# Optimization experiments

Measured on AMD Instinct MI355X. Metric: run time of the kernel, lower is better.

Reference implementation:

```python
import jax, jax.numpy as jnp
from jax import lax
import numpy as np

EPS_BN = 1e-5


def _convT(x, w, b, s, p):
    # PyTorch ConvTranspose2d(w: (Cin,Cout,k,k)) as gradient-of-conv.
    k = w.shape[2]
    wf = jnp.flip(w, (2, 3)).transpose(1, 0, 2, 3)  # (Cout,Cin,k,k)
    y = lax.conv_general_dilated(x, wf, (1, 1), [(k - 1 - p, k - 1 - p)] * 2,
                                 lhs_dilation=(s, s),
                                 dimension_numbers=('NCHW', 'OIHW', 'NCHW'))
    return y + b[None, :, None, None]


def _bn_relu(x, g, b):
    # BatchNorm2d in training mode (batch stats, biased var) + ReLU
    m = x.mean((0, 2, 3), keepdims=True)
    v = x.var((0, 2, 3), keepdims=True)
    return jax.nn.relu(g[None, :, None, None] * (x - m) * lax.rsqrt(v + EPS_BN) + b[None, :, None, None])


def _sn(w, u):
    # One power iteration (detached, as in the torch SpectralNorm impl), sigma through live w.
    wm = w.reshape(w.shape[0], -1)
    wd = lax.stop_gradient(wm)
    v = wd.T @ u
    v = v / (jnp.linalg.norm(v) + 1e-12)
    un = wd @ v
    un = un / (jnp.linalg.norm(un) + 1e-12)
    sigma = un @ (wm @ v)
    return w / sigma


def _self_attn(x, wf, bf, wg, bg, wh, bh, gamma):
    # Faithful math of Self_Attn, but without materializing the (b,C,N^2,N^2) repeat.
    b_, C, f, _ = x.shape
    N = f * f
    k = C // 8
    fx = (jnp.einsum('bchw,oc->bohw', x, wf) + bf[None, :, None, None]).reshape(b_, k, N, f, f)
    gx = (jnp.einsum('bchw,oc->bohw', x, wg) + bg[None, :, None, None]).reshape(b_, k, N, f, f)
    hx = (jnp.einsum('bchw,oc->bohw', x, wh) + bh[None, :, None, None]).reshape(b_, C, N)
    # attn_dist[b,i,a,c] = sum_k f_view[b,k,i,c,a] * g_view[b,k,i,a,c]  (f spatially transposed)
    logits = jnp.einsum('bkica,bkiac->biac', fx, gx).reshape(b_, N, N)
    attn = jax.nn.softmax(logits, axis=-1)  # (b, N, N)
    out = jnp.einsum('bcj,bij->bci', hx, attn).reshape(b_, C, f, f)
    return gamma[0] * out + x, attn[:, None]


def setup_inputs() -> dict:
    key = jax.random.key(0)
    ks = iter(jax.random.split(key, 64))

    def rn(shape, s=0.02):
        return jax.random.normal(next(ks), shape, jnp.float32) * s

    def uvec(n):
        u = jax.random.normal(next(ks), (n,), jnp.float32)
        return u / jnp.linalg.norm(u)

    B, Z = 4, 100
    d = {'z': jax.random.normal(next(ks), (B, Z), jnp.float32)}
    d.update(w1=rn((Z, 512, 4, 4)), b1=jnp.zeros(512), u1=uvec(Z), g1=jnp.ones(512), be1=jnp.zeros(512))
    d.update(w2=rn((512, 256, 4, 4)), b2=jnp.zeros(256), u2=uvec(512), g2=jnp.ones(256), be2=jnp.zeros(256))
    d.update(w3=rn((256, 128, 4, 4)), b3=jnp.zeros(128), u3=uvec(256), g3=jnp.ones(128), be3=jnp.zeros(128))
    d.update(w4=rn((128, 64, 4, 4)), b4=jnp.zeros(64), u4=uvec(128), g4=jnp.ones(64), be4=jnp.zeros(64))
    d.update(wl=rn((64, 3, 4, 4)), bl=jnp.zeros(3))
    d.update(wf1=rn((4096, 128)), bf1=jnp.zeros(4096), wg1=rn((4096, 128)), bg1=jnp.zeros(4096),
             wh1=rn((128, 128)), bh1=jnp.zeros(128), gamma1=jnp.full((1,), 0.5, jnp.float32))
    d.update(wf2=rn((8192, 64)), bf2=jnp.zeros(8192), wg2=rn((8192, 64)), bg2=jnp.zeros(8192),
             wh2=rn((64, 64)), bh2=jnp.zeros(64), gamma2=jnp.full((1,), 0.5, jnp.float32))
    return d


def reference(z, w1, b1, u1, g1, be1, w2, b2, u2, g2, be2, w3, b3, u3, g3, be3,
              w4, b4, u4, g4, be4, wl, bl,
              wf1, bf1, wg1, bg1, wh1, bh1, gamma1,
              wf2, bf2, wg2, bg2, wh2, bh2, gamma2):
    x = z[:, :, None, None]                                   # (B,100,1,1)
    x = _bn_relu(_convT(x, _sn(w1, u1), b1, 1, 0), g1, be1)   # (B,512,4,4)
    x = _bn_relu(_convT(x, _sn(w2, u2), b2, 2, 1), g2, be2)   # (B,256,8,8)
    x = _bn_relu(_convT(x, _sn(w3, u3), b3, 2, 1), g3, be3)   # (B,128,16,16)
    x, p1 = _self_attn(x, wf1, bf1, wg1, bg1, wh1, bh1, gamma1)
    x = _bn_relu(_convT(x, _sn(w4, u4), b4, 2, 1), g4, be4)   # (B,64,32,32)
    x, p2 = _self_attn(x, wf2, bf2, wg2, bg2, wh2, bh2, gamma2)
    out = jnp.tanh(_convT(x, wl, bl, 2, 1))                   # (B,3,64,64)
    return out, p1, p2
```

## Files before the change

kernel.cpp:

```cpp
#include <hip/hip_runtime.h>
#include <math.h>

#define DEV __device__ __forceinline__
typedef unsigned short ushort;
typedef __attribute__((ext_vector_type(8))) short bf16x8;
typedef __attribute__((ext_vector_type(4))) float f32x4;

constexpr int ACC   = 0;
constexpr int VR1   = 16;
constexpr int VR2   = VR1 + 8192;
constexpr int VR3   = VR2 + 4096;
constexpr int VR4   = VR3 + 2048;
constexpr int WS_Y1  = 16384;
constexpr int WS_Y2  = WS_Y1 + 32768;
constexpr int WS_Y3  = WS_Y2 + 65536;
constexpr int WS_BF3 = WS_Y3 + 131072;
constexpr int WS_H1T = WS_BF3 + 131072;
constexpr int WS_X3B = WS_H1T + 131072;
constexpr int WS_Y4  = WS_X3B + 131072;
constexpr int WS_BF4 = WS_Y4 + 262144;
constexpr int WS_H2T = WS_BF4 + 262144;
constexpr int WS_X4B = WS_H2T + 262144;
constexpr int WS_WB  = WS_X4B + 262144;
constexpr int WS_PART= WS_WB + 1048576;
constexpr int WS_WT2 = WS_PART + 1048576;
constexpr int WS_WT3 = WS_WT2 + 2097152;
constexpr int WS_WT4 = WS_WT3 + 524288;
constexpr int WS_WTL = WS_WT4 + 131072;

constexpr int O_P1 = 49152;
constexpr int O_P2 = O_P1 + 262144;

DEV ushort f2bf(float v){
  unsigned b = __float_as_uint(v);
  return (ushort)((b + 0x7fffu + ((b >> 16) & 1u)) >> 16);
}
DEV float wave_sum(float v){
  #pragma unroll
  for (int o = 32; o; o >>= 1) v += __shfl_xor(v, o, 64);
  return v;
}
DEV float wave_max(float v){
  #pragma unroll
  for (int o = 32; o; o >>= 1) v = fmaxf(v, __shfl_xor(v, o, 64));
  return v;
}
template<int T>
DEV float block_sum(float v, float* sm){
  v = wave_sum(v);
  if (T == 64) return v;
  __syncthreads();
  if ((threadIdx.x & 63) == 0) sm[threadIdx.x >> 6] = v;
  __syncthreads();
  float r = 0.f;
  #pragma unroll
  for (int i = 0; i < T/64; ++i) r += sm[i];
  return r;
}
template<int T>
DEV float block_max(float v, float* sm){
  v = wave_max(v);
  if (T == 64) return v;
  __syncthreads();
  if ((threadIdx.x & 63) == 0) sm[threadIdx.x >> 6] = v;
  __syncthreads();
  float r = -INFINITY;
  #pragma unroll
  for (int i = 0; i < T/64; ++i) r = fmaxf(r, sm[i]);
  return r;
}

DEV float inv_sigma(const float* __restrict__ ws, int wi){
  float d1 = sqrtf(ws[ACC + wi]) + 1e-12f;
  float s2 = ws[ACC + 4 + wi] / (d1 * d1);
  float sig = s2 / (sqrtf(s2) + 1e-12f);
  return 1.0f / sig;
}

__global__ void zero_vr_k(float* ws){
  int tid = blockIdx.x * 256 + threadIdx.x;
  ws[VR1 + tid] = 0.f;
  if (blockIdx.x == 0 && threadIdx.x < 8) ws[ACC + threadIdx.x] = 0.f;
}

__global__ void sn1_k(const float* __restrict__ w1, const float* __restrict__ w2,
                      const float* __restrict__ w3, const float* __restrict__ w4,
                      const float* __restrict__ u1, const float* __restrict__ u2,
                      const float* __restrict__ u3, const float* __restrict__ u4,
                      float* __restrict__ ws){
  int gid = blockIdx.x * 256 + threadIdx.x;
  int col_g = gid % 15360;
  int rchunk = gid / 15360;
  const float* W; const float* U; int rows, cols, col, voff;
  if (col_g < 8192)       { W=w1; U=u1; rows=100; cols=8192; col=col_g;        voff=VR1; }
  else if (col_g < 12288) { W=w2; U=u2; rows=512; cols=4096; col=col_g-8192;   voff=VR2; }
  else if (col_g < 14336) { W=w3; U=u3; rows=256; cols=2048; col=col_g-12288;  voff=VR3; }
  else                    { W=w4; U=u4; rows=128; cols=1024; col=col_g-14336;  voff=VR4; }
  int rc = rows >> 2;
  int r0 = rchunk * rc, r1 = r0 + rc;
  float a0=0.f, a1=0.f, a2=0.f, a3=0.f;
  int i = r0;
  for (; i + 3 < r1; i += 4){
    a0 = fmaf(W[(i  )*cols + col], U[i  ], a0);
    a1 = fmaf(W[(i+1)*cols + col], U[i+1], a1);
    a2 = fmaf(W[(i+2)*cols + col], U[i+2], a2);
    a3 = fmaf(W[(i+3)*cols + col], U[i+3], a3);
  }
  for (; i < r1; ++i) a0 = fmaf(W[i*cols + col], U[i], a0);
  atomicAdd(&ws[voff + col], (a0+a1)+(a2+a3));
}

__global__ void s1red_k(float* __restrict__ ws){
  int gid = blockIdx.x * 256 + threadIdx.x;
  int wi = gid < 8192 ? 0 : gid < 12288 ? 1 : gid < 14336 ? 2 : 3;
  float v = ws[VR1 + gid];
  float sq = wave_sum(v * v);
  if ((threadIdx.x & 63) == 0) atomicAdd(&ws[ACC + wi], sq);
}

__global__ void sn2_k(const float* __restrict__ w1, const float* __restrict__ w2,
                      const float* __restrict__ w3, const float* __restrict__ w4,
                      float* __restrict__ ws){
  int wave = (blockIdx.x * 256 + threadIdx.x) >> 6;
  int lane = threadIdx.x & 63;
  if (wave >= 996) return;
  const float* W; int row, cols, wi, voff;
  if (wave < 100)      { W=w1; row=wave;     cols=8192; wi=0; voff=VR1; }
  else if (wave < 612) { W=w2; row=wave-100; cols=4096; wi=1; voff=VR2; }
  else if (wave < 868) { W=w3; row=wave-612; cols=2048; wi=2; voff=VR3; }
  else                 { W=w4; row=wave-868; cols=1024; wi=3; voff=VR4; }
  const float* Wr = W + (size_t)row * cols;
  const float* Vr = ws + voff;
  float p0=0.f, p1=0.f, p2=0.f, p3=0.f;
  for (int j = lane; j < cols; j += 256){
    p0 = fmaf(Wr[j      ], Vr[j      ], p0);
    p1 = fmaf(Wr[j +  64], Vr[j +  64], p1);
    p2 = fmaf(Wr[j + 128], Vr[j + 128], p2);
    p3 = fmaf(Wr[j + 192], Vr[j + 192], p3);
  }
  float t = wave_sum((p0+p1)+(p2+p3));
  if (lane == 0) atomicAdd(&ws[ACC + 4 + wi], t * t);
}

__global__ void wtrans_k(const float* __restrict__ w2, const float* __restrict__ w3,
                         const float* __restrict__ w4, const float* __restrict__ wl,
                         const float* __restrict__ ws,
                         float* __restrict__ wt2, float* __restrict__ wt3,
                         float* __restrict__ wt4, float* __restrict__ wtl){
  int t = blockIdx.x * 256 + threadIdx.x;
  const float* src; float* dst; int CI, CO, loc; float inv;
  if (t < 2097152)      { src=w2; dst=wt2; CI=512; CO=256; loc=t;         inv=inv_sigma(ws,1); }
  else if (t < 2621440) { src=w3; dst=wt3; CI=256; CO=128; loc=t-2097152; inv=inv_sigma(ws,2); }
  else if (t < 2752512) { src=w4; dst=wt4; CI=128; CO=64;  loc=t-2621440; inv=inv_sigma(ws,3); }
  else                  { src=wl; dst=wtl; CI=64;  CO=3;   loc=t-2752512; inv=1.f; }
  int e  = loc & 3;
  int q  = loc >> 2;
  int co = q % CO;
  int ci = (q / CO) % CI;
  int p  = q / (CO * CI);
  int kh = (1 - (p >> 1)) + 2 * (e >> 1);
  int kw = (1 - (p & 1))  + 2 * (e & 1);
  dst[loc] = src[(ci*CO + co)*16 + kh*4 + kw] * inv;
}

__global__ void cvt_w_k(const float* __restrict__ a0, const float* __restrict__ a1,
                        const float* __restrict__ a2, const float* __restrict__ a3,
                        ushort* __restrict__ dst){
  int tid = blockIdx.x * 256 + threadIdx.x;
  int seg = tid >> 19;
  int off = tid & 524287;
  const float* s = seg == 0 ? a0 : seg == 1 ? a1 : seg == 2 ? a2 : a3;
  dst[tid] = f2bf(s[off]);
}

__global__ void conv1_k(const float* __restrict__ z, const float* __restrict__ w,
                        const float* __restrict__ bias, const float* __restrict__ ws,
                        float* __restrict__ y){
  int tid = blockIdx.x * 256 + threadIdx.x;
  int s  = tid & 15;
  int co = (tid >> 4) & 511;
  int b  = tid >> 13;
  float inv = inv_sigma(ws, 0);
  const float* zb = z + b*100;
  const float* wp = w + co*16 + s;
  float a0=0.f, a1=0.f, a2=0.f, a3=0.f;
  for (int ci = 0; ci < 100; ci += 4){
    a0 = fmaf(zb[ci  ], wp[(ci  )*8192], a0);
    a1 = fmaf(zb[ci+1], wp[(ci+1)*8192], a1);
    a2 = fmaf(zb[ci+2], wp[(ci+2)*8192], a2);
    a3 = fmaf(zb[ci+3], wp[(ci+3)*8192], a3);
  }
  y[tid] = ((a0+a1)+(a2+a3)) * inv + bias[co];
}

template<int CI, int CO, int IH>
__global__ __launch_bounds__(256) void convt_par_k(const float* __restrict__ x,
                                                   const float* __restrict__ wt,
                                                   float* __restrict__ partial){
  constexpr int OH   = 2 * IH;
  constexpr int TPJ  = 4 * IH * IH;
  constexpr int CIS  = CI / 4;
  constexpr int OUTS = 4 * CO * OH * OH;
  int tid = blockIdx.x * 256 + threadIdx.x;
  int within = tid % TPJ;
  int job    = tid / TPJ;
  int co = job % CO;
  int p  = (job / CO) & 3;
  int sc = job / (CO * 4);
  co = __builtin_amdgcn_readfirstlane(co);
  p  = __builtin_amdgcn_readfirstlane(p);
  sc = __builtin_amdgcn_readfirstlane(sc);
  int b  = within / (IH * IH);
  int rc = within % (IH * IH);
  int r = rc / IH, c = rc % IH;
  int po = p >> 1, pw = p & 1;
  int ih0 = r + po, ih1 = ih0 - 1;
  int iw0 = c + pw, iw1 = iw0 - 1;
  bool vh0 = ih0 < IH, vh1 = ih1 >= 0;
  bool vw0 = iw0 < IH, vw1 = iw1 >= 0;
  int jh0 = vh0 ? ih0 : 0, jh1 = vh1 ? ih1 : 0;
  int jw0 = vw0 ? iw0 : 0, jw1 = vw1 ? iw1 : 0;
  int o00 = jh0*IH + jw0, o01 = jh0*IH + jw1;
  int o10 = jh1*IH + jw0, o11 = jh1*IH + jw1;
  const float* xb = x + (b*CI + sc*CIS) * IH * IH;
  const float* wp = wt + (size_t)((p*CI + sc*CIS)*CO + co) * 4;
  float a00=0.f, a01=0.f, a10=0.f, a11=0.f;
  #pragma unroll 4
  for (int ci = 0; ci < CIS; ++ci){
    f32x4 wv = *(const f32x4*)(wp + (size_t)ci*CO*4);
    const float* xp = xb + ci*IH*IH;
    a00 = fmaf(xp[o00], wv[0], a00);
    a01 = fmaf(xp[o01], wv[1], a01);
    a10 = fmaf(xp[o10], wv[2], a10);
    a11 = fmaf(xp[o11], wv[3], a11);
  }
  float res = (vh0 && vw0 ? a00 : 0.f) + (vh0 && vw1 ? a01 : 0.f)
            + (vh1 && vw0 ? a10 : 0.f) + (vh1 && vw1 ? a11 : 0.f);
  int oh = 2*r + po, ow = 2*c + pw;
  partial[(size_t)sc*OUTS + ((b*CO + co)*OH + oh)*OH + ow] = res;
}

__global__ void tanh_comb_k(const float* __restrict__ partial,
                            const float* __restrict__ bl, float* __restrict__ out){
  int tid = blockIdx.x * 256 + threadIdx.x;
  int co = (tid >> 12) % 3;
  float a = partial[tid] + partial[49152 + tid] + partial[2*49152 + tid]
          + partial[3*49152 + tid] + bl[co];
  out[tid] = tanhf(a);
}

template<int C, int HW, int EPT, int THREADS>
__global__ void bn_relu_k(float* __restrict__ y, const float* __restrict__ g,
                          const float* __restrict__ be){
  __shared__ float sm[8];
  int c = blockIdx.x;
  int t = threadIdx.x;
  constexpr int N = 4 * HW;
  float v[EPT];
  #pragma unroll
  for (int k = 0; k < EPT; ++k){
    int e = t + k * THREADS;
    int b = e / HW, hw = e % HW;
    v[k] = y[(b*C + c)*HW + hw];
  }
  float s = 0.f;
  #pragma unroll
  for (int k = 0; k < EPT; ++k) s += v[k];
  s = block_sum<THREADS>(s, sm);
  float m = s / (float)N;
  float q = 0.f;
  #pragma unroll
  for (int k = 0; k < EPT; ++k){ float d = v[k] - m; q = fmaf(d, d, q); }
  q = block_sum<THREADS>(q, sm);
  float rstd = rsqrtf(q / (float)N + 1e-5f);
  float gg = g[c] * rstd, bb = be[c];
  #pragma unroll
  for (int k = 0; k < EPT; ++k){
    int e = t + k * THREADS;
    int b = e / HW, hw = e % HW;
    y[(b*C + c)*HW + hw] = fmaxf(fmaf(v[k] - m, gg, bb), 0.f);
  }
}

template<int C, int HW, int EPT, int THREADS>
__global__ void bn_relu_sum_k(const float* __restrict__ partial,
                              const float* __restrict__ bias,
                              const float* __restrict__ g, const float* __restrict__ be,
                              float* __restrict__ y){
  __shared__ float sm[8];
  constexpr int OUTS = 4 * C * HW;
  int c = blockIdx.x;
  int t = threadIdx.x;
  constexpr int N = 4 * HW;
  float cb = bias[c];
  float v[EPT];
  #pragma unroll
  for (int k = 0; k < EPT; ++k){
    int e = t + k * THREADS;
    int b = e / HW, hw = e % HW;
    int idx = (b*C + c)*HW + hw;
    v[k] = partial[idx] + partial[OUTS + idx] + partial[2*OUTS + idx]
         + partial[3*OUTS + idx] + cb;
  }
  float s = 0.f;
  #pragma unroll
  for (int k = 0; k < EPT; ++k) s += v[k];
  s = block_sum<THREADS>(s, sm);
  float m = s / (float)N;
  float q = 0.f;
  #pragma unroll
  for (int k = 0; k < EPT; ++k){ float d = v[k] - m; q = fmaf(d, d, q); }
  q = block_sum<THREADS>(q, sm);
  float rstd = rsqrtf(q / (float)N + 1e-5f);
  float gg = g[c] * rstd, bb = be[c];
  #pragma unroll
  for (int k = 0; k < EPT; ++k){
    int e = t + k * THREADS;
    int b = e / HW, hw = e % HW;
    y[(b*C + c)*HW + hw] = fmaxf(fmaf(v[k] - m, gg, bb), 0.f);
  }
}

template<int C, int F>
__global__ void prep_attn_k(const float* __restrict__ x, const float* __restrict__ wh,
                            const float* __restrict__ bh,
                            ushort* __restrict__ xs, ushort* __restrict__ xts,
                            float* __restrict__ ht){
  constexpr int N = F * F;
  constexpr int G1 = (4 * C * N) / 256;
  int blk = blockIdx.x;
  if (blk < G1){
    int tid = blk * 256 + threadIdx.x;
    int c = tid % C;
    int s = (tid / C) % N;
    int b = tid / (C * N);
    xs[tid]  = f2bf(x[(b*C + c)*N + s]);
    int ts = (s % F) * F + s / F;
    xts[tid] = f2bf(x[(b*C + c)*N + ts]);
  } else {
    int tid = (blk - G1) * 256 + threadIdx.x;
    int j  = tid % N;
    int cc = (tid / N) % C;
    int b  = tid / (N*C);
    float a = bh[cc];
    for (int ch = 0; ch < C; ++ch)
      a = fmaf(wh[cc*C + ch], x[(b*C + ch)*N + j], a);
    ht[(b*N + j)*C + cc] = a;
  }
}

template<int C, int N, int K, int JPB>
__global__ __launch_bounds__(256) void logits_mfma_res_k(
    const ushort* __restrict__ xs, const ushort* __restrict__ xts,
    const ushort* __restrict__ wfb, const ushort* __restrict__ wgb,
    const float* __restrict__ bfp, const float* __restrict__ bgp,
    float* __restrict__ out){
  constexpr int NF  = C / 32;
  constexpr int NIG = N / 64;
  constexpr int NJC = (N / 16) / JPB;
  int w = threadIdx.x >> 6, l = threadIdx.x & 63;
  int lr = l & 15, lg = l >> 4;
  int blk = blockIdx.x;
  int jc = blk % NJC;
  int ib = (blk / NJC) % NIG;
  int b  = blk / (NJC * NIG);
  int i0 = ib * 64 + w * 16;
  int j0 = jc * (JPB * 16);

  bf16x8 af[K][NF], ag[K][NF];
  f32x4 bfv[K], bgv[K];
  #pragma unroll
  for (int kk = 0; kk < K; ++kk){
    #pragma unroll
    for (int f = 0; f < NF; ++f){
      int ro = (kk*N + i0 + lr)*C + f*32 + lg*8;
      af[kk][f] = *(const bf16x8*)(wfb + ro);
      ag[kk][f] = *(const bf16x8*)(wgb + ro);
    }
    bfv[kk] = *(const f32x4*)(bfp + kk*N + i0 + lg*4);
    bgv[kk] = *(const f32x4*)(bgp + kk*N + i0 + lg*4);
  }
  const ushort* xsp  = xs  + (b*N + j0 + lr)*C + lg*8;
  const ushort* xtsp = xts + (b*N + j0 + lr)*C + lg*8;
  float* op = out + (size_t)(b*N + i0 + lg*4)*N + j0 + lr;
  for (int it = 0; it < JPB; ++it){
    bf16x8 bs[NF], bt[NF];
    #pragma unroll
    for (int f = 0; f < NF; ++f){
      bs[f] = *(const bf16x8*)(xsp  + it*16*C + f*32);
      bt[f] = *(const bf16x8*)(xtsp + it*16*C + f*32);
    }
    f32x4 acc = {0.f, 0.f, 0.f, 0.f};
    #pragma unroll
    for (int kk = 0; kk < K; ++kk){
      f32x4 F = bfv[kk], G = bgv[kk];
      #pragma unroll
      for (int f = 0; f < NF; ++f){
        F = __builtin_amdgcn_mfma_f32_16x16x32_bf16(af[kk][f], bt[f], F, 0, 0, 0);
        G = __builtin_amdgcn_mfma_f32_16x16x32_bf16(ag[kk][f], bs[f], G, 0, 0, 0);
      }
      #pragma unroll
      for (int r = 0; r < 4; ++r) acc[r] = fmaf(F[r], G[r], acc[r]);
    }
    #pragma unroll
    for (int r = 0; r < 4; ++r) op[(size_t)r*N + it*16] = acc[r];
  }
}

template<int C, int N, int K, int JPB>
__global__ __launch_bounds__(256) void logits_mfma_split_k(
    const ushort* __restrict__ xs, const ushort* __restrict__ xts,
    const ushort* __restrict__ wfb, const ushort* __restrict__ wgb,
    const float* __restrict__ bfp, const float* __restrict__ bgp,
    float* __restrict__ out){
  constexpr int NF  = C / 32;
  constexpr int KW  = K / 4;
  constexpr int NJC = (N / 16) / JPB;
  __shared__ float red[3][320];
  int w = threadIdx.x >> 6, l = threadIdx.x & 63;
  int lr = l & 15, lg = l >> 4;
  int blk = blockIdx.x;
  int jc = blk % NJC;
  int ig = (blk / NJC) % (N / 16);
  int b  = blk / (NJC * (N / 16));
  int i0 = ig * 16;
  int j0 = jc * (JPB * 16);
  int k0 = w * KW;

  bf16x8 af[KW][NF], ag[KW][NF];
  f32x4 bfv[KW], bgv[KW];
  #pragma unroll
  for (int kk = 0; kk < KW; ++kk){
    #pragma unroll
    for (int f = 0; f < NF; ++f){
      int ro = ((k0 + kk)*N + i0 + lr)*C + f*32 + lg*8;
      af[kk][f] = *(const bf16x8*)(wfb + ro);
      ag[kk][f] = *(const bf16x8*)(wgb + ro);
    }
    bfv[kk] = *(const f32x4*)(bfp + (k0 + kk)*N + i0 + lg*4);
    bgv[kk] = *(const f32x4*)(bgp + (k0 + kk)*N + i0 + lg*4);
  }
  const ushort* xsp  = xs  + (b*N + j0 + lr)*C + lg*8;
  const ushort* xtsp = xts + (b*N + j0 + lr)*C + lg*8;
  float* op = out + (size_t)(b*N + i0 + lg*4)*N + j0 + lr;
  for (int it = 0; it < JPB; ++it){
    bf16x8 bs[NF], bt[NF];
    #pragma unroll
    for (int f = 0; f < NF; ++f){
      bs[f] = *(const bf16x8*)(xsp  + it*16*C + f*32);
      bt[f] = *(const bf16x8*)(xtsp + it*16*C + f*32);
    }
    f32x4 acc = {0.f, 0.f, 0.f, 0.f};
    #pragma unroll
    for (int kk = 0; kk < KW; ++kk){
      f32x4 F = bfv[kk], G = bgv[kk];
      #pragma unroll
      for (int f = 0; f < NF; ++f){
        F = __builtin_amdgcn_mfma_f32_16x16x32_bf16(af[kk][f], bt[f], F, 0, 0, 0);
        G = __builtin_amdgcn_mfma_f32_16x16x32_bf16(ag[kk][f], bs[f], G, 0, 0, 0);
      }
      #pragma unroll
      for (int r = 0; r < 4; ++r) acc[r] = fmaf(F[r], G[r], acc[r]);
    }
    if (w > 0){
      #pragma unroll
      for (int r = 0; r < 4; ++r) red[w-1][l*5 + r] = acc[r];
    }
    __syncthreads();
    if (w == 0){
      #pragma unroll
      for (int ww = 0; ww < 3; ++ww)
        #pragma unroll
        for (int r = 0; r < 4; ++r) acc[r] += red[ww][l*5 + r];
      #pragma unroll
      for (int r = 0; r < 4; ++r) op[(size_t)r*N + it*16] = acc[r];
    }
    __syncthreads();
  }
}

template<int LEN, int EPT>
__global__ void softmax_k(float* __restrict__ p){
  __shared__ float sm[8];
  int row = blockIdx.x;
  int t = threadIdx.x;
  float v[EPT];
  #pragma unroll
  for (int k = 0; k < EPT; ++k) v[k] = p[row*LEN + t + k*256];
  float m = -INFINITY;
  #pragma unroll
  for (int k = 0; k < EPT; ++k) m = fmaxf(m, v[k]);
  m = block_max<256>(m, sm);
  float s = 0.f;
  #pragma unroll
  for (int k = 0; k < EPT; ++k){ v[k] = expf(v[k] - m); s += v[k]; }
  s = block_sum<256>(s, sm);
  #pragma unroll
  for (int k = 0; k < EPT; ++k) p[row*LEN + t + k*256] = v[k] / s;
}

template<int C, int N, int IL>
__global__ void attnout_k(const float* __restrict__ ht, const float* __restrict__ attn,
                          const float* __restrict__ x, const float* __restrict__ gamma,
                          float* __restrict__ xo){
  int tid = blockIdx.x * 256 + threadIdx.x;
  int cc = tid % C;
  int ig = (tid / C) % (N / IL);
  int b  = tid / (C * (N / IL));
  int i0 = ig * IL;
  const float* hb = ht + b*N*C + cc;
  const float* ar = attn + (size_t)(b*N + i0) * N;
  float acc[IL];
  #pragma unroll
  for (int il = 0; il < IL; ++il) acc[il] = 0.f;
  for (int jj = 0; jj < N; ++jj){
    float h = hb[jj*C];
    #pragma unroll
    for (int il = 0; il < IL; ++il)
      acc[il] = fmaf(ar[il*N + jj], h, acc[il]);
  }
  float gm = gamma[0];
  #pragma unroll
  for (int il = 0; il < IL; ++il){
    int xi = (b*C + cc)*N + i0 + il;
    xo[xi] = fmaf(gm, acc[il], x[xi]);
  }
}

extern "C" void kernel_launch(void* const* d_in, const int* in_sizes, int n_in,
                              void* d_out, int out_size, void* d_ws, size_t ws_size,
                              hipStream_t stream){
  const float* z   = (const float*)d_in[0];
  const float* w1  = (const float*)d_in[1];  const float* b1  = (const float*)d_in[2];
  const float* u1  = (const float*)d_in[3];  const float* g1  = (const float*)d_in[4];
  const float* be1 = (const float*)d_in[5];
  const float* w2  = (const float*)d_in[6];  const float* b2  = (const float*)d_in[7];
  const float* u2  = (const float*)d_in[8];  const float* g2  = (const float*)d_in[9];
  const float* be2 = (const float*)d_in[10];
  const float* w3  = (const float*)d_in[11]; const float* b3  = (const float*)d_in[12];
  const float* u3  = (const float*)d_in[13]; const float* g3  = (const float*)d_in[14];
  const float* be3 = (const float*)d_in[15];
  const float* w4  = (const float*)d_in[16]; const float* b4  = (const float*)d_in[17];
  const float* u4  = (const float*)d_in[18]; const float* g4  = (const float*)d_in[19];
  const float* be4 = (const float*)d_in[20];
  const float* wl  = (const float*)d_in[21]; const float* bl  = (const float*)d_in[22];
  const float* wf1 = (const float*)d_in[23]; const float* bf1 = (const float*)d_in[24];
  const float* wg1 = (const float*)d_in[25]; const float* bg1 = (const float*)d_in[26];
  const float* wh1 = (const float*)d_in[27]; const float* bh1 = (const float*)d_in[28];
  const float* gamma1 = (const float*)d_in[29];
  const float* wf2 = (const float*)d_in[30]; const float* bf2 = (const float*)d_in[31];
  const float* wg2 = (const float*)d_in[32]; const float* bg2 = (const float*)d_in[33];
  const float* wh2 = (const float*)d_in[34]; const float* bh2 = (const float*)d_in[35];
  const float* gamma2 = (const float*)d_in[36];

  float* ws  = (float*)d_ws;
  float* out = (float*)d_out;

  ushort* wb    = (ushort*)(ws + WS_WB);
  ushort* wf1b  = wb;
  ushort* wg1b  = wb + 524288;
  ushort* wf2b  = wb + 2*524288;
  ushort* wg2b  = wb + 3*524288;
  ushort* xs3   = (ushort*)(ws + WS_BF3);
  ushort* xts3  = xs3 + 131072;
  ushort* xs4   = (ushort*)(ws + WS_BF4);
  ushort* xts4  = xs4 + 262144;
  float*  part  = ws + WS_PART;

  zero_vr_k<<<60, 256, 0, stream>>>(ws);
  sn1_k<<<240, 256, 0, stream>>>(w1, w2, w3, w4, u1, u2, u3, u4, ws);
  s1red_k<<<60, 256, 0, stream>>>(ws);
  sn2_k<<<249, 256, 0, stream>>>(w1, w2, w3, w4, ws);
  wtrans_k<<<10764, 256, 0, stream>>>(w2, w3, w4, wl, ws,
                                      ws + WS_WT2, ws + WS_WT3, ws + WS_WT4, ws + WS_WTL);
  cvt_w_k<<<8192, 256, 0, stream>>>(wf1, wg1, wf2, wg2, wb);

  conv1_k<<<128, 256, 0, stream>>>(z, w1, b1, ws, ws + WS_Y1);
  bn_relu_k<512, 16, 1, 64><<<512, 64, 0, stream>>>(ws + WS_Y1, g1, be1);

  convt_par_k<512, 256, 4><<<1024, 256, 0, stream>>>(ws + WS_Y1, ws + WS_WT2, part);
  bn_relu_sum_k<256, 64, 1, 256><<<256, 256, 0, stream>>>(part, b2, g2, be2, ws + WS_Y2);

  convt_par_k<256, 128, 8><<<2048, 256, 0, stream>>>(ws + WS_Y2, ws + WS_WT3, part);
  bn_relu_sum_k<128, 256, 4, 256><<<128, 256, 0, stream>>>(part, b3, g3, be3, ws + WS_Y3);

  prep_attn_k<128, 16><<<1024, 256, 0, stream>>>(ws + WS_Y3, wh1, bh1,
                                                 xs3, xts3, ws + WS_H1T);
  logits_mfma_split_k<128, 256, 16, 4><<<256, 256, 0, stream>>>(
      xs3, xts3, wf1b, wg1b, bf1, bg1, out + O_P1);
  softmax_k<256, 1><<<1024, 256, 0, stream>>>(out + O_P1);
  attnout_k<128, 256, 4><<<128, 256, 0, stream>>>(ws + WS_H1T, out + O_P1, ws + WS_Y3,
                                                  gamma1, ws + WS_X3B);

  convt_par_k<128, 64, 16><<<4096, 256, 0, stream>>>(ws + WS_X3B, ws + WS_WT4, part);
  bn_relu_sum_k<64, 1024, 16, 256><<<64, 256, 0, stream>>>(part, b4, g4, be4, ws + WS_Y4);

  prep_attn_k<64, 32><<<2048, 256, 0, stream>>>(ws + WS_Y4, wh2, bh2,
                                                xs4, xts4, ws + WS_H2T);
  logits_mfma_res_k<64, 1024, 8, 8><<<512, 256, 0, stream>>>(
      xs4, xts4, wf2b, wg2b, bf2, bg2, out + O_P2);
  softmax_k<1024, 4><<<4096, 256, 0, stream>>>(out + O_P2);
  attnout_k<64, 1024, 4><<<256, 256, 0, stream>>>(ws + WS_H2T, out + O_P2, ws + WS_Y4,
                                                  gamma2, ws + WS_X4B);

  convt_par_k<64, 3, 32><<<768, 256, 0, stream>>>(ws + WS_X4B, ws + WS_WTL, part);
  tanh_comb_k<<<192, 256, 0, stream>>>(part, bl, out);
}
```

Baseline: 420.4 us.

## Split attention-output reduction over keys into partial and combine kernels

Replaces the single attention-output kernel with a split-K variant that divides the j (key) loop into JS chunks. Each chunk writes partial sums to a scratch buffer placed over the early weight-transpose workspace region, and a second kernel sums the partials and applies the gamma residual. This multiplies the number of launched blocks so more of the device has work on the long serial reduction. In exchange it adds an extra launch and partial-sum traffic through global memory. It also relies on that reused workspace region no longer being needed.

Result: no change. 413.3 us (-1.7%).

```diff
diff --git a/kernel.cpp b/kernel.cpp
--- a/kernel.cpp
+++ b/kernel.cpp
@@ -499,32 +499,54 @@
   for (int k = 0; k < EPT; ++k) p[row*LEN + t + k*256] = v[k] / s;
 }
 
-template<int C, int N, int IL>
-__global__ void attnout_k(const float* __restrict__ ht, const float* __restrict__ attn,
-                          const float* __restrict__ x, const float* __restrict__ gamma,
-                          float* __restrict__ xo){
+template<int C, int N, int IL, int JS>
+__global__ void attnout_split_k(const float* __restrict__ ht,
+                                const float* __restrict__ attn,
+                                float* __restrict__ partial){
+  constexpr int NIG = N / IL;
+  constexpr int JC  = N / JS;
+  constexpr int SZ  = 4 * C * N;
   int tid = blockIdx.x * 256 + threadIdx.x;
   int cc = tid % C;
-  int ig = (tid / C) % (N / IL);
-  int b  = tid / (C * (N / IL));
+  int ig = (tid / C) % NIG;
+  int js = (tid / (C * NIG)) % JS;
+  int b  = tid / (C * NIG * JS);
   int i0 = ig * IL;
-  const float* hb = ht + b*N*C + cc;
-  const float* ar = attn + (size_t)(b*N + i0) * N;
+  int j0 = js * JC;
+  const float* hb = ht + (size_t)(b*N + j0)*C + cc;
+  const float* ar = attn + (size_t)(b*N + i0)*N + j0;
   float acc[IL];
   #pragma unroll
   for (int il = 0; il < IL; ++il) acc[il] = 0.f;
-  for (int jj = 0; jj < N; ++jj){
-    float h = hb[jj*C];
+  #pragma unroll 8
+  for (int jj = 0; jj < JC; ++jj){
+    float h = hb[(size_t)jj*C];
     #pragma unroll
     for (int il = 0; il < IL; ++il)
-      acc[il] = fmaf(ar[il*N + jj], h, acc[il]);
-  }
-  float gm = gamma[0];
-  #pragma unroll
-  for (int il = 0; il < IL; ++il){
-    int xi = (b*C + cc)*N + i0 + il;
-    xo[xi] = fmaf(gm, acc[il], x[xi]);
-  }
+      acc[il] = fmaf(ar[(size_t)il*N + jj], h, acc[il]);
+  }
+  float* pp = partial + (size_t)js*SZ + ((size_t)(b*NIG + ig)*C + cc)*IL;
+  #pragma unroll
+  for (int il = 0; il < IL; ++il) pp[il] = acc[il];
+}
+
+template<int C, int N, int IL, int JS>
+__global__ void attnout_comb_k(const float* __restrict__ partial,
+                               const float* __restrict__ x,
+                               const float* __restrict__ gamma,
+                               float* __restrict__ xo){
+  constexpr int NIG = N / IL;
+  constexpr int SZ  = 4 * C * N;
+  int tid = blockIdx.x * 256 + threadIdx.x;
+  int i  = tid % N;
+  int cc = (tid / N) % C;
+  int b  = tid / (N * C);
+  int ig = i / IL, il = i % IL;
+  size_t pidx = ((size_t)(b*NIG + ig)*C + cc)*IL + il;
+  float s = 0.f;
+  #pragma unroll
+  for (int js = 0; js < JS; ++js) s += partial[(size_t)js*SZ + pidx];
+  xo[tid] = fmaf(gamma[0], s, x[tid]);
 }
 
 extern "C" void kernel_launch(void* const* d_in, const int* in_sizes, int n_in,
@@ -566,6 +588,7 @@
   ushort* xs4   = (ushort*)(ws + WS_BF4);
   ushort* xts4  = xs4 + 262144;
   float*  part  = ws + WS_PART;
+  float*  part2 = ws + WS_WT2;
 
   zero_vr_k<<<60, 256, 0, stream>>>(ws);
   sn1_k<<<240, 256, 0, stream>>>(w1, w2, w3, w4, u1, u2, u3, u4, ws);
@@ -589,8 +612,9 @@
   logits_mfma_split_k<128, 256, 16, 4><<<256, 256, 0, stream>>>(
       xs3, xts3, wf1b, wg1b, bf1, bg1, out + O_P1);
   softmax_k<256, 1><<<1024, 256, 0, stream>>>(out + O_P1);
-  attnout_k<128, 256, 4><<<128, 256, 0, stream>>>(ws + WS_H1T, out + O_P1, ws + WS_Y3,
-                                                  gamma1, ws + WS_X3B);
+  attnout_split_k<128, 256, 4, 4><<<512, 256, 0, stream>>>(ws + WS_H1T, out + O_P1, part2);
+  attnout_comb_k<128, 256, 4, 4><<<512, 256, 0, stream>>>(part2, ws + WS_Y3, gamma1,
+                                                          ws + WS_X3B);
 
   convt_par_k<128, 64, 16><<<4096, 256, 0, stream>>>(ws + WS_X3B, ws + WS_WT4, part);
   bn_relu_sum_k<64, 1024, 16, 256><<<64, 256, 0, stream>>>(part, b4, g4, be4, ws + WS_Y4);
@@ -600,8 +624,9 @@
   logits_mfma_res_k<64, 1024, 8, 8><<<512, 256, 0, stream>>>(
       xs4, xts4, wf2b, wg2b, bf2, bg2, out + O_P2);
   softmax_k<1024, 4><<<4096, 256, 0, stream>>>(out + O_P2);
-  attnout_k<64, 1024, 4><<<256, 256, 0, stream>>>(ws + WS_H2T, out + O_P2, ws + WS_Y4,
-                                                  gamma2, ws + WS_X4B);
+  attnout_split_k<64, 1024, 4, 8><<<2048, 256, 0, stream>>>(ws + WS_H2T, out + O_P2, part2);
+  attnout_comb_k<64, 1024, 4, 8><<<1024, 256, 0, stream>>>(part2, ws + WS_Y4, gamma2,
+                                                           ws + WS_X4B);
 
   convt_par_k<64, 3, 32><<<768, 256, 0, stream>>>(ws + WS_X4B, ws + WS_WTL, part);
   tanh_comb_k<<<192, 256, 0, stream>>>(part, bl, out);
```

## Compute attention output with bf16 MFMA and split-K partial reduction

Applied to the files above, without the earlier changes.

Replaces the scalar fp32 attention-output kernel with an MFMA kernel that consumes bf16 copies of the softmax probabilities and h-projection. Softmax now also writes a bf16 copy of the probabilities, and prep_attn writes h in channel-major bf16. A split-K partial sum is reduced in a separate finalize kernel that adds the gamma-scaled residual. This trades fp32 accuracy for bf16 and adds extra writes and a kernel launch, and reuses a workspace region for the bf16 probabilities.

Result: faster. 373.3 us (-11.2%).

```diff
diff --git a/kernel.cpp b/kernel.cpp
--- a/kernel.cpp
+++ b/kernel.cpp
@@ -325,7 +325,7 @@
 __global__ void prep_attn_k(const float* __restrict__ x, const float* __restrict__ wh,
                             const float* __restrict__ bh,
                             ushort* __restrict__ xs, ushort* __restrict__ xts,
-                            float* __restrict__ ht){
+                            ushort* __restrict__ hb){
   constexpr int N = F * F;
   constexpr int G1 = (4 * C * N) / 256;
   int blk = blockIdx.x;
@@ -345,7 +345,7 @@
     float a = bh[cc];
     for (int ch = 0; ch < C; ++ch)
       a = fmaf(wh[cc*C + ch], x[(b*C + ch)*N + j], a);
-    ht[(b*N + j)*C + cc] = a;
+    hb[tid] = f2bf(a);
   }
 }
 
@@ -480,7 +480,7 @@
 }
 
 template<int LEN, int EPT>
-__global__ void softmax_k(float* __restrict__ p){
+__global__ void softmax_k(float* __restrict__ p, ushort* __restrict__ pb){
   __shared__ float sm[8];
   int row = blockIdx.x;
   int t = threadIdx.x;
@@ -496,35 +496,58 @@
   for (int k = 0; k < EPT; ++k){ v[k] = expf(v[k] - m); s += v[k]; }
   s = block_sum<256>(s, sm);
   #pragma unroll
-  for (int k = 0; k < EPT; ++k) p[row*LEN + t + k*256] = v[k] / s;
-}
-
-template<int C, int N, int IL>
-__global__ void attnout_k(const float* __restrict__ ht, const float* __restrict__ attn,
-                          const float* __restrict__ x, const float* __restrict__ gamma,
-                          float* __restrict__ xo){
+  for (int k = 0; k < EPT; ++k){
+    float r = v[k] / s;
+    p[row*LEN + t + k*256]  = r;
+    pb[row*LEN + t + k*256] = f2bf(r);
+  }
+}
+
+template<int C, int N, int KS>
+__global__ __launch_bounds__(256) void attnout_mfma_k(
+    const ushort* __restrict__ pb, const ushort* __restrict__ hb,
+    float* __restrict__ partial){
+  constexpr int NIT = N / 16;
+  constexpr int NCT = C / 16;
+  constexpr int KC  = N / KS;
+  constexpr int NKF = KC / 32;
+  constexpr int SZ  = 4 * C * N;
+  int w = threadIdx.x >> 6, l = threadIdx.x & 63;
+  int lr = l & 15, lg = l >> 4;
+  int wid = blockIdx.x * 4 + w;
+  int ks  = wid % KS;
+  int cct = (wid / KS) % NCT;
+  int it  = (wid / (KS * NCT)) % NIT;
+  int b   = wid / (KS * NCT * NIT);
+  int koff = ks * KC;
+
+  const ushort* pp = pb + (size_t)(b*N + it*16 + lr)*N + koff + lg*8;
+  bf16x8 bfr[NKF];
+  #pragma unroll
+  for (int f = 0; f < NKF; ++f) bfr[f] = *(const bf16x8*)(pp + f*32);
+  const ushort* hp = hb + (size_t)(b*C + cct*16 + lr)*N + koff + lg*8;
+  f32x4 acc = {0.f, 0.f, 0.f, 0.f};
+  #pragma unroll
+  for (int f = 0; f < NKF; ++f){
+    bf16x8 afr = *(const bf16x8*)(hp + f*32);
+    acc = __builtin_amdgcn_mfma_f32_16x16x32_bf16(afr, bfr[f], acc, 0, 0, 0);
+  }
+  float* op = partial + (size_t)ks*SZ + ((size_t)(b*C + cct*16 + lg*4)*N + it*16 + lr);
+  #pragma unroll
+  for (int r = 0; r < 4; ++r) op[(size_t)r*N] = acc[r];
+}
+
+template<int C, int N, int KS>
+__global__ void attnout_fin_k(const float* __restrict__ partial,
+                              const float* __restrict__ x,
+                              const float* __restrict__ gamma,
+                              float* __restrict__ xo){
+  constexpr int SZ = 4 * C * N;
   int tid = blockIdx.x * 256 + threadIdx.x;
-  int cc = tid % C;
-  int ig = (tid / C) % (N / IL);
-  int b  = tid / (C * (N / IL));
-  int i0 = ig * IL;
-  const float* hb = ht + b*N*C + cc;
-  const float* ar = attn + (size_t)(b*N + i0) * N;
-  float acc[IL];
-  #pragma unroll
-  for (int il = 0; il < IL; ++il) acc[il] = 0.f;
-  for (int jj = 0; jj < N; ++jj){
-    float h = hb[jj*C];
-    #pragma unroll
-    for (int il = 0; il < IL; ++il)
-      acc[il] = fmaf(ar[il*N + jj], h, acc[il]);
-  }
-  float gm = gamma[0];
-  #pragma unroll
-  for (int il = 0; il < IL; ++il){
-    int xi = (b*C + cc)*N + i0 + il;
-    xo[xi] = fmaf(gm, acc[il], x[xi]);
-  }
+  float s = 0.f;
+  #pragma unroll
+  for (int ks = 0; ks < KS; ++ks) s += partial[(size_t)ks*SZ + tid];
+  xo[tid] = fmaf(gamma[0], s, x[tid]);
 }
 
 extern "C" void kernel_launch(void* const* d_in, const int* in_sizes, int n_in,
@@ -565,6 +588,9 @@
   ushort* xts3  = xs3 + 131072;
   ushort* xs4   = (ushort*)(ws + WS_BF4);
   ushort* xts4  = xs4 + 262144;
+  ushort* hb1   = (ushort*)(ws + WS_H1T);
+  ushort* hb2   = (ushort*)(ws + WS_H2T);
+  ushort* pbuf  = (ushort*)(ws + WS_WT2);
   float*  part  = ws + WS_PART;
 
   zero_vr_k<<<60, 256, 0, stream>>>(ws);
@@ -584,24 +610,24 @@
   convt_par_k<256, 128, 8><<<2048, 256, 0, stream>>>(ws + WS_Y2, ws + WS_WT3, part);
   bn_relu_sum_k<128, 256, 4, 256><<<128, 256, 0, stream>>>(part, b3, g3, be3, ws + WS_Y3);
 
-  prep_attn_k<128, 16><<<1024, 256, 0, stream>>>(ws + WS_Y3, wh1, bh1,
-                                                 xs3, xts3, ws + WS_H1T);
+  prep_attn_k<128, 16><<<1024, 256, 0, stream>>>(ws + WS_Y3, wh1, bh1, xs3, xts3, hb1);
   logits_mfma_split_k<128, 256, 16, 4><<<256, 256, 0, stream>>>(
       xs3, xts3, wf1b, wg1b, bf1, bg1, out + O_P1);
-  softmax_k<256, 1><<<1024, 256, 0, stream>>>(out + O_P1);
-  attnout_k<128, 256, 4><<<128, 256, 0, stream>>>(ws + WS_H1T, out + O_P1, ws + WS_Y3,
-                                                  gamma1, ws + WS_X3B);
+  softmax_k<256, 1><<<1024, 256, 0, stream>>>(out + O_P1, pbuf);
+  attnout_mfma_k<128, 256, 1><<<128, 256, 0, stream>>>(pbuf, hb1, part);
+  attnout_fin_k<128, 256, 1><<<512, 256, 0, stream>>>(part, ws + WS_Y3, gamma1,
+                                                      ws + WS_X3B);
 
   convt_par_k<128, 64, 16><<<4096, 256, 0, stream>>>(ws + WS_X3B, ws + WS_WT4, part);
   bn_relu_sum_k<64, 1024, 16, 256><<<64, 256, 0, stream>>>(part, b4, g4, be4, ws + WS_Y4);
 
-  prep_attn_k<64, 32><<<2048, 256, 0, stream>>>(ws + WS_Y4, wh2, bh2,
-                                                xs4, xts4, ws + WS_H2T);
+  prep_attn_k<64, 32><<<2048, 256, 0, stream>>>(ws + WS_Y4, wh2, bh2, xs4, xts4, hb2);
   logits_mfma_res_k<64, 1024, 8, 8><<<512, 256, 0, stream>>>(
       xs4, xts4, wf2b, wg2b, bf2, bg2, out + O_P2);
-  softmax_k<1024, 4><<<4096, 256, 0, stream>>>(out + O_P2);
-  attnout_k<64, 1024, 4><<<256, 256, 0, stream>>>(ws + WS_H2T, out + O_P2, ws + WS_Y4,
-                                                  gamma2, ws + WS_X4B);
+  softmax_k<1024, 4><<<4096, 256, 0, stream>>>(out + O_P2, pbuf);
+  attnout_mfma_k<64, 1024, 4><<<1024, 256, 0, stream>>>(pbuf, hb2, part);
+  attnout_fin_k<64, 1024, 4><<<1024, 256, 0, stream>>>(part, ws + WS_Y4, gamma2,
+                                                       ws + WS_X4B);
 
   convt_par_k<64, 3, 32><<<768, 256, 0, stream>>>(ws + WS_X4B, ws + WS_WTL, part);
   tanh_comb_k<<<192, 256, 0, stream>>>(part, bl, out);
```
